# Optimization experiments

Measured on AMD Instinct MI355X. Metric: run time of the kernel, lower is better.

The kernel has to match this reference:

```python
import jax, jax.numpy as jnp
import numpy as np

B, N, P, E = 4096, 1024, 32, 16  # batch, generator dim, n_params, expand_ratio


def setup_inputs() -> dict:
    key = jax.random.key(0)
    k1, k2, k3 = jax.random.split(key, 3)
    x = jax.random.normal(k1, (B, N), dtype=jnp.float32)
    # params ~ stdv*rand - stdv as in the module (stdv=0.01)
    params = 0.01 * jax.random.uniform(k2, (P, E), dtype=jnp.float32) - 0.01
    transformations = jax.random.normal(k3, (P, N, N), dtype=jnp.float32)
    return {"x": x, "params": params, "transformations": transformations}


def reference(x, params, transformations):
    # Fused version of the per-dim loop in ExpandFilterFunctionNew2:
    # filter_e = (params[:, e] @ transformations.flatten(1)).reshape(N, N)
    P_, N_, _ = transformations.shape
    E_ = params.shape[-1]
    filters = jnp.einsum('pe,pq->eq', params, transformations.reshape(P_, -1))
    filters = filters.reshape(E_, N_, N_)              # [E, N, N]
    # output[b, i, e] = sum_j filter[e, i, j] * x[b, j]
    out = jnp.einsum('eij,bj->bie', filters, x)        # [B, N, E]
    # Swish activation (add_linear=False path)
    return out * jax.nn.sigmoid(out)
```

## Files before the change

kernel.cpp:

```cpp
#include <hip/hip_runtime.h>
#include <hip/hip_bf16.h>
#include <stdint.h>

#define BB 4096
#define NN 1024
#define PP 32
#define EE 16
#define NC (NN*EE)

typedef __bf16 bf16x8 __attribute__((ext_vector_type(8)));
typedef float  f32x4  __attribute__((ext_vector_type(4)));

__device__ __forceinline__ void gl2lds16(const void* g, void* l) {
  __builtin_amdgcn_global_load_lds(
      (const __attribute__((address_space(1))) void*)g,
      (__attribute__((address_space(3))) void*)l,
      16, 0, 0);
}

__global__ __launch_bounds__(256) void cvt_x_kernel(
    const float* __restrict__ x, __hip_bfloat16* __restrict__ xb) {
  size_t i4 = (size_t)blockIdx.x * 256 + threadIdx.x;
  float4 v = ((const float4*)x)[i4];
  union { __hip_bfloat16 h[4]; ushort4 u; } pk;
  pk.h[0] = __float2bfloat16(v.x);
  pk.h[1] = __float2bfloat16(v.y);
  pk.h[2] = __float2bfloat16(v.z);
  pk.h[3] = __float2bfloat16(v.w);
  *(ushort4*)(xb + i4 * 4) = pk.u;
}

__global__ __launch_bounds__(256) void make_filters(
    const float* __restrict__ params,
    const float* __restrict__ T,
    __hip_bfloat16* __restrict__ Gt) {
  const int tid = threadIdx.x;
  const int i = blockIdx.x;
  const int j = tid * 4;
  const float4* Tv = (const float4*)T;
  const size_t qv = ((size_t)i * NN + j) >> 2;

  float acc[EE][4];
#pragma unroll
  for (int e = 0; e < EE; ++e) {
    acc[e][0] = 0.f; acc[e][1] = 0.f; acc[e][2] = 0.f; acc[e][3] = 0.f;
  }

  for (int p = 0; p < PP; ++p) {
    float4 t = Tv[(size_t)p * (NN * NN / 4) + qv];
#pragma unroll
    for (int e = 0; e < EE; ++e) {
      float w = params[p * EE + e];
      acc[e][0] += w * t.x; acc[e][1] += w * t.y;
      acc[e][2] += w * t.z; acc[e][3] += w * t.w;
    }
  }

#pragma unroll
  for (int e = 0; e < EE; ++e) {
    union { __hip_bfloat16 h[4]; ushort4 u; } pk;
    pk.h[0] = __float2bfloat16(acc[e][0]);
    pk.h[1] = __float2bfloat16(acc[e][1]);
    pk.h[2] = __float2bfloat16(acc[e][2]);
    pk.h[3] = __float2bfloat16(acc[e][3]);
    *(ushort4*)&Gt[((size_t)i * EE + e) * NN + j] = pk.u;
  }
}

__global__ __launch_bounds__(256) void gemm_swish(
    const __hip_bfloat16* __restrict__ A,
    const __hip_bfloat16* __restrict__ Bt,
    float* __restrict__ C) {
  __shared__ __hip_bfloat16 As[128 * 32];
  __shared__ __hip_bfloat16 Bs[128 * 32];

  const int tid  = threadIdx.x;
  const int bn   = blockIdx.x;
  const int bm   = blockIdx.y;
  const int wv   = tid >> 6;
  const int lane = tid & 63;

  const int ldrow = tid >> 2;
  const int ldcol = (tid & 3) * 8;
  const __hip_bfloat16* a0 = A  + ((size_t)bm * 128 + ldrow) * NN + ldcol;
  const __hip_bfloat16* b0 = Bt + ((size_t)bn * 128 + ldrow) * NN + ldcol;
  char* asDst = (char*)As + wv * 1024;
  char* bsDst = (char*)Bs + wv * 1024;

  const int wm   = (wv >> 1) * 64;
  const int wn   = (wv & 1) * 64;
  const int lrow = lane & 15;
  const int lk   = (lane >> 4) * 8;

  f32x4 acc[4][4] = {};

  for (int kt = 0; kt < NN / 32; ++kt) {
    const int k0 = kt * 32;
    __syncthreads();
    gl2lds16(a0 + k0,            asDst);
    gl2lds16(a0 + 64 * NN + k0,  asDst + 4096);
    gl2lds16(b0 + k0,            bsDst);
    gl2lds16(b0 + 64 * NN + k0,  bsDst + 4096);
    __syncthreads();

    bf16x8 af[4], bfr[4];
#pragma unroll
    for (int mt = 0; mt < 4; ++mt)
      af[mt] = *(const bf16x8*)&As[(wm + mt * 16 + lrow) * 32 + lk];
#pragma unroll
    for (int nt = 0; nt < 4; ++nt)
      bfr[nt] = *(const bf16x8*)&Bs[(wn + nt * 16 + lrow) * 32 + lk];

#pragma unroll
    for (int mt = 0; mt < 4; ++mt)
#pragma unroll
      for (int nt = 0; nt < 4; ++nt)
        acc[mt][nt] = __builtin_amdgcn_mfma_f32_16x16x32_bf16(
            af[mt], bfr[nt], acc[mt][nt], 0, 0, 0);
  }

  const size_t row0 = (size_t)bm * 128 + wm + (lane >> 4) * 4;
  const size_t col0 = (size_t)bn * 128 + wn + (lane & 15);
#pragma unroll
  for (int mt = 0; mt < 4; ++mt) {
#pragma unroll
    for (int nt = 0; nt < 4; ++nt) {
      const size_t col = col0 + nt * 16;
#pragma unroll
      for (int r = 0; r < 4; ++r) {
        float o = acc[mt][nt][r];
        float s = o / (1.0f + __expf(-o));
        C[(row0 + mt * 16 + r) * NC + col] = s;
      }
    }
  }
}

extern "C" void kernel_launch(void* const* d_in, const int* in_sizes, int n_in,
                              void* d_out, int out_size, void* d_ws, size_t ws_size,
                              hipStream_t stream) {
  const float* x      = (const float*)d_in[0];
  const float* params = (const float*)d_in[1];
  const float* T      = (const float*)d_in[2];
  float* out = (float*)d_out;

  __hip_bfloat16* Gt = (__hip_bfloat16*)d_ws;
  __hip_bfloat16* xb = (__hip_bfloat16*)((char*)d_ws + (size_t)NC * NN * 2);

  cvt_x_kernel<<<(BB * NN / 4) / 256, 256, 0, stream>>>(x, xb);
  make_filters<<<NN, 256, 0, stream>>>(params, T, Gt);
  gemm_swish<<<dim3(NC / 128, BB / 128), 256, 0, stream>>>(xb, Gt, out);
}
```

Baseline: 530.8 us.

## Swap MFMA operands for vectorized float4 stores, remap blocks per XCD, unroll filter loads

The GEMM epilogue now swaps the MFMA A/B operands so each lane holds four consecutive output columns, letting it write one 16-byte store per tile instead of four scalar strided stores to the large fp32 output. Block indices are remapped so consecutive blocks on the same XCD share column tiles of the filter matrix, aiming for better L2 reuse. The swish divide is replaced by a hardware reciprocal, and the filter-building loop loads four transformation slabs at once to raise memory-level parallelism. The fast reciprocal slightly reduces precision of the activation.

```diff
diff --git a/kernel.cpp b/kernel.cpp
--- a/kernel.cpp
+++ b/kernel.cpp
@@ -39,6 +39,7 @@
   const int j = tid * 4;
   const float4* Tv = (const float4*)T;
   const size_t qv = ((size_t)i * NN + j) >> 2;
+  const size_t SLABQ = (size_t)NN * NN / 4;
 
   float acc[EE][4];
 #pragma unroll
@@ -46,13 +47,25 @@
     acc[e][0] = 0.f; acc[e][1] = 0.f; acc[e][2] = 0.f; acc[e][3] = 0.f;
   }
 
-  for (int p = 0; p < PP; ++p) {
-    float4 t = Tv[(size_t)p * (NN * NN / 4) + qv];
+  for (int p = 0; p < PP; p += 4) {
+    float4 t0 = Tv[(size_t)(p + 0) * SLABQ + qv];
+    float4 t1 = Tv[(size_t)(p + 1) * SLABQ + qv];
+    float4 t2 = Tv[(size_t)(p + 2) * SLABQ + qv];
+    float4 t3 = Tv[(size_t)(p + 3) * SLABQ + qv];
 #pragma unroll
     for (int e = 0; e < EE; ++e) {
-      float w = params[p * EE + e];
-      acc[e][0] += w * t.x; acc[e][1] += w * t.y;
-      acc[e][2] += w * t.z; acc[e][3] += w * t.w;
+      float w0 = params[(p + 0) * EE + e];
+      float w1 = params[(p + 1) * EE + e];
+      float w2 = params[(p + 2) * EE + e];
+      float w3 = params[(p + 3) * EE + e];
+      acc[e][0] += w0 * t0.x; acc[e][1] += w0 * t0.y;
+      acc[e][2] += w0 * t0.z; acc[e][3] += w0 * t0.w;
+      acc[e][0] += w1 * t1.x; acc[e][1] += w1 * t1.y;
+      acc[e][2] += w1 * t1.z; acc[e][3] += w1 * t1.w;
+      acc[e][0] += w2 * t2.x; acc[e][1] += w2 * t2.y;
+      acc[e][2] += w2 * t2.z; acc[e][3] += w2 * t2.w;
+      acc[e][0] += w3 * t3.x; acc[e][1] += w3 * t3.y;
+      acc[e][2] += w3 * t3.z; acc[e][3] += w3 * t3.w;
     }
   }
 
@@ -75,8 +88,13 @@
   __shared__ __hip_bfloat16 Bs[128 * 32];
 
   const int tid  = threadIdx.x;
-  const int bn   = blockIdx.x;
-  const int bm   = blockIdx.y;
+
+  const int flat = blockIdx.y * 128 + blockIdx.x;
+  const int xcd  = flat & 7;
+  const int idx  = flat >> 3;
+  const int bm   = idx & 31;
+  const int bn   = xcd * 16 + (idx >> 5);
+
   const int wv   = tid >> 6;
   const int lane = tid & 63;
 
@@ -116,22 +134,24 @@
 #pragma unroll
       for (int nt = 0; nt < 4; ++nt)
         acc[mt][nt] = __builtin_amdgcn_mfma_f32_16x16x32_bf16(
-            af[mt], bfr[nt], acc[mt][nt], 0, 0, 0);
+            bfr[nt], af[mt], acc[mt][nt], 0, 0, 0);
   }
 
-  const size_t row0 = (size_t)bm * 128 + wm + (lane >> 4) * 4;
-  const size_t col0 = (size_t)bn * 128 + wn + (lane & 15);
+  const size_t row0 = (size_t)bm * 128 + wm + (lane & 15);
+  const size_t col0 = (size_t)bn * 128 + wn + (lane >> 4) * 4;
 #pragma unroll
   for (int mt = 0; mt < 4; ++mt) {
+    const size_t rbase = (row0 + mt * 16) * (size_t)NC;
 #pragma unroll
     for (int nt = 0; nt < 4; ++nt) {
-      const size_t col = col0 + nt * 16;
+      f32x4 v = acc[mt][nt];
+      f32x4 s;
 #pragma unroll
       for (int r = 0; r < 4; ++r) {
-        float o = acc[mt][nt][r];
-        float s = o / (1.0f + __expf(-o));
-        C[(row0 + mt * 16 + r) * NC + col] = s;
+        float o = v[r];
+        s[r] = o * __builtin_amdgcn_rcpf(1.0f + __expf(-o));
       }
+      *(f32x4*)&C[rbase + col0 + nt * 16] = s;
     }
   }
 }
```

New measurement: 584.6 us. 10.1% more time.
